# Performance work log

Hardware: AMD Instinct MI355X
Metric: run time of the kernel (lower is better)

Reference implementation:

```python
import jax, jax.numpy as jnp
import numpy as np

HEAD_SIZE = 128
N_Q_HEADS = 32
N_KV_HEADS = 8
ROPE_THETA = 1000000.0
RMS_EPS = 1e-6


def rms_norm(x, w, eps=RMS_EPS):
    # normalize over last dim in fp32, like Qwen3RMSNorm
    xf = x.astype(jnp.float32)
    var = jnp.mean(xf * xf, axis=-1, keepdims=True)
    return w * (xf * jax.lax.rsqrt(var + eps)).astype(x.dtype)


def rope_cache(T, dim, theta=ROPE_THETA):
    half = dim // 2
    inv_freq = 1.0 / theta ** (jnp.arange(half, dtype=jnp.float32) / half)
    freqs = jnp.arange(T, dtype=jnp.float32)[:, None] * inv_freq[None, :]  # [T, half]
    emb = jnp.concatenate([freqs, freqs], axis=-1)  # [T, dim]
    return jnp.cos(emb), jnp.sin(emb)


def rotate_half(x):
    x1, x2 = jnp.split(x, 2, axis=-1)
    return jnp.concatenate([-x2, x1], axis=-1)


def setup_inputs() -> dict:
    key = jax.random.key(0)
    ks = jax.random.split(key, 5)
    B, T, C = 2, 2048, 4096
    s = 0.02
    return {
        "hidden_states": jax.random.normal(ks[0], (B, T, C), jnp.float32),
        "wq": jax.random.normal(ks[1], (N_Q_HEADS * HEAD_SIZE, C), jnp.float32) * s,
        "wk": jax.random.normal(ks[2], (N_KV_HEADS * HEAD_SIZE, C), jnp.float32) * s,
        "wv": jax.random.normal(ks[3], (N_KV_HEADS * HEAD_SIZE, C), jnp.float32) * s,
        "wo": jax.random.normal(ks[4], (C, N_Q_HEADS * HEAD_SIZE), jnp.float32) * s,
        "q_norm_w": jnp.ones((HEAD_SIZE,), jnp.float32),
        "k_norm_w": jnp.ones((HEAD_SIZE,), jnp.float32),
    }


def reference(hidden_states, wq, wk, wv, wo, q_norm_w, k_norm_w):
    B, T, C = hidden_states.shape
    D = HEAD_SIZE
    groups = N_Q_HEADS // N_KV_HEADS
    scale = D ** -0.5

    # projections -> [B, H, T, D]
    q = (hidden_states @ wq.T).reshape(B, T, N_Q_HEADS, D)
    k = (hidden_states @ wk.T).reshape(B, T, N_KV_HEADS, D)
    v = (hidden_states @ wv.T).reshape(B, T, N_KV_HEADS, D)

    q = rms_norm(q, q_norm_w).transpose(0, 2, 1, 3)
    k = rms_norm(k, k_norm_w).transpose(0, 2, 1, 3)
    v = v.transpose(0, 2, 1, 3)

    cos, sin = rope_cache(T, D)  # [T, D]
    cos = cos[None, None]  # broadcast over batch, heads
    sin = sin[None, None]
    q = q * cos + rotate_half(q) * sin
    k = k * cos + rotate_half(k) * sin

    # GQA repeat_kv: [B, Hkv, T, D] -> [B, Hq, T, D]
    k = jnp.repeat(k, groups, axis=1)
    v = jnp.repeat(v, groups, axis=1)

    # causal SDPA
    scores = jnp.einsum("bhqd,bhkd->bhqk", q, k) * scale
    causal = jnp.tril(jnp.ones((T, T), bool))
    scores = jnp.where(causal[None, None], scores, -jnp.inf)
    probs = jax.nn.softmax(scores, axis=-1)
    attn = jnp.einsum("bhqk,bhkd->bhqd", probs, v)

    attn = attn.transpose(0, 2, 1, 3).reshape(B, T, N_Q_HEADS * D)
    return attn @ wo.T
```

## Files before the change

kernel.cpp:

```cpp
#include <hip/hip_runtime.h>
#include <math.h>

typedef unsigned short u16;
typedef __attribute__((ext_vector_type(8))) short short8;
typedef __attribute__((ext_vector_type(4))) float f32x4;
typedef __attribute__((ext_vector_type(16))) float f32x16;

#define AS1 __attribute__((address_space(1)))
#define AS3 __attribute__((address_space(3)))

__device__ __forceinline__ void gload_lds16(const u16* g, u16* l) {
  __builtin_amdgcn_global_load_lds((AS1 void*)g, (AS3 void*)l, 16, 0, 0);
}

__device__ __forceinline__ float bf2f(u16 u) {
  union { unsigned i; float f; } c; c.i = ((unsigned)u) << 16; return c.f;
}
__device__ __forceinline__ u16 f2bf(float f) {
  union { float f; unsigned i; } c; c.f = f;
  unsigned r = c.i + 0x7fffu + ((c.i >> 16) & 1u);
  return (u16)(r >> 16);
}

__global__ __launch_bounds__(256)
void cvt_f32_bf16_k(const float* __restrict__ src, u16* __restrict__ dst, int n8)
{
  int i = blockIdx.x * blockDim.x + threadIdx.x;
  const int stride = gridDim.x * blockDim.x;
  for (; i < n8; i += stride) {
    float4 a = ((const float4*)src)[2 * i];
    float4 b = ((const float4*)src)[2 * i + 1];
    short8 o;
    o[0] = (short)f2bf(a.x); o[1] = (short)f2bf(a.y);
    o[2] = (short)f2bf(a.z); o[3] = (short)f2bf(a.w);
    o[4] = (short)f2bf(b.x); o[5] = (short)f2bf(b.y);
    o[6] = (short)f2bf(b.z); o[7] = (short)f2bf(b.w);
    ((short8*)dst)[i] = o;
  }
}

__global__ __launch_bounds__(256)
void cvt_batch4(const float* __restrict__ s0, u16* __restrict__ d0,
                const float* __restrict__ s1, u16* __restrict__ d1,
                const float* __restrict__ s2, u16* __restrict__ d2,
                const float* __restrict__ s3, u16* __restrict__ d3)
{
  int i = blockIdx.x * blockDim.x + threadIdx.x;
  const int stride = gridDim.x * blockDim.x;
  for (; i < 5242880; i += stride) {
    const float* s; u16* d; int j;
    if (i < 2097152)      { s = s0; d = d0; j = i; }
    else if (i < 4194304) { s = s1; d = d1; j = i - 2097152; }
    else if (i < 4718592) { s = s2; d = d2; j = i - 4194304; }
    else                  { s = s3; d = d3; j = i - 4718592; }
    float4 a = ((const float4*)s)[2 * j];
    float4 b = ((const float4*)s)[2 * j + 1];
    short8 o;
    o[0] = (short)f2bf(a.x); o[1] = (short)f2bf(a.y);
    o[2] = (short)f2bf(a.z); o[3] = (short)f2bf(a.w);
    o[4] = (short)f2bf(b.x); o[5] = (short)f2bf(b.y);
    o[6] = (short)f2bf(b.z); o[7] = (short)f2bf(b.w);
    ((short8*)d)[j] = o;
  }
}

#define MFMA16(a, b, c) __builtin_amdgcn_mfma_f32_16x16x32_bf16((a), (b), (c), 0, 0, 0)

#define STAGE_H(panel, h, t, ldsb)                                          \
  { const u16* s_ = (panel) + (size_t)((h) * 128) * 4096 + (t) * 64;        \
    gload_lds16(s_,                   (ldsb) + ldst0);                      \
    gload_lds16(s_ + (size_t)64*4096, (ldsb) + 4096 + ldst0); }

#define PHASE(MB, STAGE_STMT, TAIL)                                         \
  {                                                                         \
    short8 a0k0 = *(const short8*)(aB + (MB)*1024 + aoff0);                 \
    short8 a0k1 = *(const short8*)(aB + (MB)*1024 + (aoff0 ^ 32));          \
    short8 a1k0 = *(const short8*)(aB + ((MB)+1)*1024 + aoff0);             \
    short8 a1k1 = *(const short8*)(aB + ((MB)+1)*1024 + (aoff0 ^ 32));      \
    __builtin_amdgcn_s_barrier();                                           \
    asm volatile("s_waitcnt lgkmcnt(0)" ::: "memory");                      \
    __builtin_amdgcn_s_setprio(1);                                          \
    _Pragma("unroll")                                                       \
    for (int n = 0; n < 4; ++n) {                                           \
      acc[(MB)][n]   = MFMA16(a0k0, br[n][0], acc[(MB)][n]);                \
      acc[(MB)][n]   = MFMA16(a0k1, br[n][1], acc[(MB)][n]);                \
      acc[(MB)+1][n] = MFMA16(a1k0, br[n][0], acc[(MB)+1][n]);              \
      acc[(MB)+1][n] = MFMA16(a1k1, br[n][1], acc[(MB)+1][n]);              \
    }                                                                       \
    __builtin_amdgcn_s_setprio(0);                                          \
    STAGE_STMT                                                              \
    TAIL                                                                    \
  }

#define KTILE(BUF, T)                                                       \
  {                                                                         \
    const u16* aB = sA + (BUF) * 16384 + wr * 8192;                         \
    const u16* bB = sB + (BUF) * 16384 + (wc >> 1) * 8192;                  \
    u16* aO = sA + ((BUF) ^ 1) * 16384;                                     \
    u16* bO = sB + (BUF) * 16384;                                           \
    const bool st1 = (T) + 1 < NT, st2 = (T) + 2 < NT;                      \
    short8 br[4][2];                                                        \
    _Pragma("unroll")                                                       \
    for (int n = 0; n < 4; ++n) {                                           \
      br[n][0] = *(const short8*)(bB + n * 1024 + boff0);                   \
      br[n][1] = *(const short8*)(bB + n * 1024 + (boff0 ^ 32));            \
    }                                                                       \
    PHASE(0, if (st1) STAGE_H(aS, 0, (T) + 1, aO);, ;)                      \
    PHASE(2, if (st1) STAGE_H(aS, 1, (T) + 1, aO + 8192);, ;)               \
    PHASE(4, if (st2) STAGE_H(bS, 0, (T) + 2, bO);, ;)                      \
    PHASE(6, if (st2) STAGE_H(bS, 1, (T) + 2, bO + 8192);,                  \
          if ((T) < NT - 2) { asm volatile("s_waitcnt vmcnt(4)" ::: "memory"); } \
          else              { asm volatile("s_waitcnt vmcnt(0)" ::: "memory"); } \
          __builtin_amdgcn_s_barrier();)                                    \
  }

template<int MODE, typename OutT>
__global__ __launch_bounds__(512, 2)
void gemm256(const u16* __restrict__ A, const u16* __restrict__ W0,
             const u16* __restrict__ W1, const u16* __restrict__ W2,
             OutT* __restrict__ C)
{
  constexpr int K = 4096;
  constexpr int NT = K / 64;
  constexpr int LDC = (MODE == 0) ? 6144 : 4096;
  constexpr int NBM = 16;
  constexpr int NBN = (MODE == 0) ? 24 : 16;
  constexpr int NWG = NBM * NBN;

  __shared__ __align__(16) u16 sA[2 * 16384];
  __shared__ __align__(16) u16 sB[2 * 16384];

  const int tid = threadIdx.x;
  const int wid = tid >> 6, lane = tid & 63;
  const int g = lane >> 4, li = lane & 15;
  const int wr = wid >> 2, wc = wid & 3;

  const int bid = blockIdx.x;
  const int wg = (bid & 7) * (NWG / 8) + (bid >> 3);
  const int bm = wg % NBM, bn = wg / NBM;
  const int n0 = bn * 256;

  const u16* Wp; int nrow0;
  if (MODE == 0) {
    if (n0 < 4096)      { Wp = W0; nrow0 = n0; }
    else if (n0 < 5120) { Wp = W1; nrow0 = n0 - 4096; }
    else                { Wp = W2; nrow0 = n0 - 5120; }
  } else { Wp = W0; nrow0 = n0; }

  const int r0 = tid >> 3;
  const int sc0 = (tid & 7) ^ (r0 & 7);
  const u16* aS = A  + (size_t)(bm * 256 + r0) * K + sc0 * 8;
  const u16* bS = Wp + (size_t)(nrow0   + r0) * K + sc0 * 8;
  const int ldst0 = wid * 512;

  const int aoff0 = li * 64 + ((g ^ (li & 7)) * 8);
  const int boff0 = (wc & 1) * 4096 + aoff0;

  f32x4 acc[8][4] = {};

  STAGE_H(bS, 0, 0, sB);
  STAGE_H(bS, 1, 0, sB + 8192);
  STAGE_H(aS, 0, 0, sA);
  STAGE_H(aS, 1, 0, sA + 8192);
  STAGE_H(bS, 0, 1, sB + 16384);
  STAGE_H(bS, 1, 1, sB + 24576);
  asm volatile("s_waitcnt vmcnt(4)" ::: "memory");
  __builtin_amdgcn_s_barrier();

  for (int t = 0; t < NT; t += 2) {
    KTILE(0, t)
    KTILE(1, t + 1)
  }

#pragma unroll
  for (int m = 0; m < 8; ++m)
#pragma unroll
    for (int n = 0; n < 4; ++n)
#pragma unroll
      for (int j = 0; j < 4; ++j) {
        int row = bm * 256 + wr * 128 + m * 16 + g * 4 + j;
        int col = n0 + wc * 64 + n * 16 + li;
        float v = acc[m][n][j];
        if constexpr (sizeof(OutT) == 2) C[(size_t)row * LDC + col] = (OutT)f2bf(v);
        else                             C[(size_t)row * LDC + col] = (OutT)v;
      }
}

__global__ __launch_bounds__(256)
void norm_rope(const u16* __restrict__ qkv, const float* __restrict__ qw,
               const float* __restrict__ kw, u16* __restrict__ Qo,
               u16* __restrict__ Ko)
{
  const int tid = threadIdx.x;
  const int wid = tid >> 6, l = tid & 63;
  const int idx = blockIdx.x * 4 + wid;

  const u16* src; const float* w; u16* dst; int t;
  if (idx < 131072) {
    int row = idx >> 5, h = idx & 31;
    int b = row >> 11; t = row & 2047;
    src = qkv + (size_t)row * 6144 + h * 128;
    w = qw;
    dst = Qo + (((size_t)(b * 32 + h)) * 2048 + t) * 128;
  } else {
    int j = idx - 131072;
    int row = j >> 3, hk = j & 7;
    int b = row >> 11; t = row & 2047;
    src = qkv + (size_t)row * 6144 + 4096 + hk * 128;
    w = kw;
    dst = Ko + (((size_t)(b * 8 + hk)) * 2048 + t) * 128;
  }

  float x1 = bf2f(src[l]), x2 = bf2f(src[l + 64]);
  float ss = x1 * x1 + x2 * x2;
#pragma unroll
  for (int off = 32; off; off >>= 1) ss += __shfl_xor(ss, off);
  float rn = rsqrtf(ss * (1.0f / 128.0f) + 1e-6f);
  float y1 = x1 * rn * w[l];
  float y2 = x2 * rn * w[l + 64];

  float ang = (float)t * expf((float)l * -0.21586735246819178f);
  float c = cosf(ang), s = sinf(ang);
  dst[l]      = f2bf(y1 * c - y2 * s);
  dst[l + 64] = f2bf(y2 * c + y1 * s);
}

__global__ __launch_bounds__(256)
void transpose_v(const u16* __restrict__ qkv, u16* __restrict__ Vt)
{
  const int tblk = blockIdx.x, bh = blockIdx.y;
  const int b = bh >> 3, hk = bh & 7;
  const int tid = threadIdx.x;
  __shared__ __align__(16) u16 tile[64][136];

#pragma unroll
  for (int r = 0; r < 4; ++r) {
    int u = tid + r * 256;
    int row = u >> 4, cu = u & 15;
    short8 v = *(const short8*)(qkv + (size_t)(b * 2048 + tblk * 64 + row) * 6144
                                + 5120 + hk * 128 + cu * 8);
    *(short8*)(&tile[row][cu * 8]) = v;
  }
  __syncthreads();
#pragma unroll
  for (int it = 0; it < 4; ++it) {
    int u = tid + it * 256;
    int d = u & 127, tg = u >> 7;
    short8 wv8;
#pragma unroll
    for (int j = 0; j < 8; ++j) wv8[j] = (short)tile[tg * 8 + j][d];
    *(short8*)(Vt + ((size_t)(b * 8 + hk) * 128 + d) * 2048 + tblk * 64 + tg * 8) = wv8;
  }
}

__global__ __launch_bounds__(256, 2)
void attn_fwd(const u16* __restrict__ Q, const u16* __restrict__ Kc,
              const u16* __restrict__ Vt, u16* __restrict__ O)
{
  const int qt = 15 - (int)blockIdx.x;
  const int bh = blockIdx.y;
  const int b = bh >> 5, h = bh & 31, hkv = h >> 2;
  const int tid = threadIdx.x, wid = tid >> 6;
  const int lane = tid & 63, ql = lane & 31, hi = lane >> 5;

  __shared__ __align__(16) u16 sK[2][64 * 128];
  __shared__ __align__(16) u16 sV[2][128 * 64];

  const u16* Kb = Kc + ((size_t)(b * 8 + hkv)) * 2048 * 128;
  const u16* Vb = Vt + ((size_t)(b * 8 + hkv)) * 128 * 2048;

  const int kr0 = tid >> 4;
  const u16* kSrc = Kb + (size_t)kr0 * 128 + (((tid & 15) ^ (kr0 & 7)) * 8);
  const int vr0 = tid >> 3;
  const u16* vSrc = Vb + (size_t)vr0 * 2048 + (((tid & 7) ^ (vr0 & 7)) * 8);
  u16* const kDst = (u16*)sK[0] + wid * 512;
  u16* const vDst = (u16*)sV[0] + wid * 512;

  const int qg = qt * 128 + wid * 32 + ql;
  const u16* qrow = Q + ((size_t)(b * 32 + h) * 2048 + qg) * 128;
  short8 qf[8];
#pragma unroll
  for (int m = 0; m < 8; ++m) qf[m] = *(const short8*)(qrow + m * 16 + hi * 8);

  f32x16 oacc[4] = {};
  float mrun = -INFINITY, lrun = 0.f;
  const float scale = 0.08838834764831845f;
  const int nt = 2 * qt + 2;

#pragma unroll
  for (int p = 0; p < 4; ++p) {
    gload_lds16(kSrc + p * 2048,  kDst + p * 2048);
    gload_lds16(vSrc + p * 65536, vDst + p * 2048);
  }
  asm volatile("s_waitcnt vmcnt(0)" ::: "memory");
  __builtin_amdgcn_s_barrier();

  int cur = 0;
  for (int kt = 0; kt < nt; ++kt) {
    const int kv0 = kt * 64;
    if (kt + 1 < nt) {
      const u16* ks = kSrc + (size_t)(kv0 + 64) * 128;
      const u16* vs = vSrc + (kv0 + 64);
      u16* kd = kDst + (cur ^ 1) * 8192;
      u16* vd = vDst + (cur ^ 1) * 8192;
#pragma unroll
      for (int p = 0; p < 4; ++p) {
        gload_lds16(ks + p * 2048,  kd + p * 2048);
        gload_lds16(vs + p * 65536, vd + p * 2048);
      }
    }
    const u16* sKc = sK[cur];
    const u16* sVc = sV[cur];

    f32x16 P0 = {}, P1 = {};
    __builtin_amdgcn_s_setprio(1);
#pragma unroll
    for (int m = 0; m < 8; ++m) {
      const int c0 = ((m * 2 + hi) ^ (ql & 7)) * 8;
      short8 k0 = *(const short8*)(sKc + ql * 128 + c0);
      short8 k1 = *(const short8*)(sKc + (32 + ql) * 128 + c0);
      P0 = __builtin_amdgcn_mfma_f32_32x32x16_bf16(k0, qf[m], P0, 0, 0, 0);
      P1 = __builtin_amdgcn_mfma_f32_32x32x16_bf16(k1, qf[m], P1, 0, 0, 0);
    }
    __builtin_amdgcn_s_setprio(0);

#pragma unroll
    for (int r = 0; r < 16; ++r) {
      const int kvl = (r & 3) + 8 * (r >> 2) + 4 * hi;
      float v0 = P0[r] * scale; if (kv0 + kvl > qg)      v0 = -INFINITY; P0[r] = v0;
      float v1 = P1[r] * scale; if (kv0 + 32 + kvl > qg) v1 = -INFINITY; P1[r] = v1;
    }

    float pmax = -INFINITY;
#pragma unroll
    for (int r = 0; r < 16; ++r) pmax = fmaxf(pmax, fmaxf(P0[r], P1[r]));
    pmax = fmaxf(pmax, __shfl_xor(pmax, 32));

    if (!__all(pmax - mrun <= 8.f)) {
      float mnew = fmaxf(mrun, pmax);
      float corr = __expf(mrun - mnew);
      lrun *= corr;
      mrun = mnew;
#pragma unroll
      for (int r = 0; r < 16; ++r) {
        int qidx = (r & 3) + 8 * (r >> 2) + 4 * hi;
        float cr = __shfl(corr, qidx);
#pragma unroll
        for (int dt = 0; dt < 4; ++dt) oacc[dt][r] *= cr;
      }
    }

    float psum = 0.f;
#pragma unroll
    for (int r = 0; r < 16; ++r) {
      float e0 = __expf(P0[r] - mrun); P0[r] = e0; psum += e0;
      float e1 = __expf(P1[r] - mrun); P1[r] = e1; psum += e1;
    }
    psum += __shfl_xor(psum, 32);
    lrun += psum;

    __builtin_amdgcn_s_setprio(1);
#pragma unroll
    for (int s = 0; s < 4; ++s) {
      const int R0 = 8 * (s & 1), R1 = R0 + 4;
      float a0 = (s < 2) ? P0[R0 + 0] : P1[R0 + 0];
      float a1 = (s < 2) ? P0[R0 + 1] : P1[R0 + 1];
      float a2 = (s < 2) ? P0[R0 + 2] : P1[R0 + 2];
      float a3 = (s < 2) ? P0[R0 + 3] : P1[R0 + 3];
      float b0 = (s < 2) ? P0[R1 + 0] : P1[R1 + 0];
      float b1 = (s < 2) ? P0[R1 + 1] : P1[R1 + 1];
      float b2 = (s < 2) ? P0[R1 + 2] : P1[R1 + 2];
      float b3 = (s < 2) ? P0[R1 + 3] : P1[R1 + 3];
      unsigned y0, y1, z0, z1;
      asm("v_cvt_pk_bf16_f32 %0, %1, %2" : "=v"(y0) : "v"(a0), "v"(a1));
      asm("v_cvt_pk_bf16_f32 %0, %1, %2" : "=v"(z0) : "v"(b0), "v"(b1));
      asm("v_cvt_pk_bf16_f32 %0, %1, %2" : "=v"(y1) : "v"(a2), "v"(a3));
      asm("v_cvt_pk_bf16_f32 %0, %1, %2" : "=v"(z1) : "v"(b2), "v"(b3));
      asm("v_permlane32_swap_b32 %0, %1" : "+v"(y0), "+v"(z0));
      asm("v_permlane32_swap_b32 %0, %1" : "+v"(y1), "+v"(z1));
      union { unsigned u[4]; short8 v; } pa;
      pa.u[0] = y0; pa.u[1] = y1; pa.u[2] = z0; pa.u[3] = z1;
#pragma unroll
      for (int dt = 0; dt < 4; ++dt) {
        const int c = ((s * 2 + hi) ^ (ql & 7)) * 8;
        short8 vf = *(const short8*)(sVc + (dt * 32 + ql) * 64 + c);
        oacc[dt] = __builtin_amdgcn_mfma_f32_32x32x16_bf16(pa.v, vf, oacc[dt], 0, 0, 0);
      }
    }
    __builtin_amdgcn_s_setprio(0);

    asm volatile("s_waitcnt lgkmcnt(0)" ::: "memory");
    asm volatile("s_waitcnt vmcnt(0)" ::: "memory");
    __builtin_amdgcn_s_barrier();
    cur ^= 1;
  }

  float inv = 1.f / lrun;
  const int qbase = b * 2048 + qt * 128 + wid * 32;
#pragma unroll
  for (int r = 0; r < 16; ++r) {
    const int qidx = (r & 3) + 8 * (r >> 2) + 4 * hi;
    float ir = __shfl(inv, qidx);
    size_t base = (size_t)(qbase + qidx) * 4096 + h * 128 + ql;
#pragma unroll
    for (int dt = 0; dt < 4; ++dt)
      O[base + dt * 32] = f2bf(oacc[dt][r] * ir);
  }
}

extern "C" void kernel_launch(void* const* d_in, const int* in_sizes, int n_in,
                              void* d_out, int out_size, void* d_ws, size_t ws_size,
                              hipStream_t stream) {
  const float* hs  = (const float*)d_in[0];
  const float* wq  = (const float*)d_in[1];
  const float* wk  = (const float*)d_in[2];
  const float* wv  = (const float*)d_in[3];
  const float* wo  = (const float*)d_in[4];
  const float* qnw = (const float*)d_in[5];
  const float* knw = (const float*)d_in[6];
  float* out = (float*)d_out;

  char* ws = (char*)d_ws;
  u16* qkv = (u16*)(ws);
  u16* qr  = (u16*)(ws + 50331648);
  u16* kr  = (u16*)(ws + 83886080);
  u16* vt  = (u16*)(ws + 92274688);
  u16* hsb = (u16*)(ws + 100663296);
  u16* wqb = (u16*)(ws + 134217728);
  u16* wkb = (u16*)(ws + 167772160);
  u16* wvb = (u16*)(ws + 176160768);
  u16* ao  = (u16*)(ws);
  u16* wob = hsb;

  cvt_batch4<<<dim3(2048), dim3(256), 0, stream>>>(hs, hsb, wq, wqb, wk, wkb, wv, wvb);

  gemm256<0, u16><<<dim3(384), dim3(512), 0, stream>>>(hsb, wqb, wkb, wvb, qkv);
  cvt_f32_bf16_k<<<dim3(2048), dim3(256), 0, stream>>>(wo, wob, 16777216 / 8);
  norm_rope<<<dim3(40960), dim3(256), 0, stream>>>(qkv, qnw, knw, qr, kr);
  transpose_v<<<dim3(32, 16), dim3(256), 0, stream>>>(qkv, vt);
  attn_fwd<<<dim3(16, 64), dim3(256), 0, stream>>>(qr, kr, vt, ao);

  gemm256<1, float><<<dim3(256), dim3(512), 0, stream>>>(ao, wob, nullptr, nullptr, out);
}
```

Before: 631.9 us.

## Add 128x256-tile QKV GEMM and restructure stage/barrier ordering in output GEMM

Measured after the change: 626.2 us. No clear change (-0.9%).

```diff
diff --git a/kernel.cpp b/kernel.cpp
--- a/kernel.cpp
+++ b/kernel.cpp
@@ -66,6 +66,130 @@
 
 #define MFMA16(a, b, c) __builtin_amdgcn_mfma_f32_16x16x32_bf16((a), (b), (c), 0, 0, 0)
 
+#define QSTG_A(t, bufb)                                                     \
+  { const u16* s_ = aS + (size_t)(t) * 64;                                  \
+    gload_lds16(s_,                     sA + (bufb) + ldst0);               \
+    gload_lds16(s_ + (size_t)64 * 4096, sA + (bufb) + 4096 + ldst0); }
+
+#define QSTG_B(t, bufb)                                                     \
+  { const u16* s_ = bS + (size_t)(t) * 64;                                  \
+    gload_lds16(s_,                      sB + (bufb) + ldst0);              \
+    gload_lds16(s_ + (size_t)64 * 4096,  sB + (bufb) + 4096 + ldst0);       \
+    gload_lds16(s_ + (size_t)128 * 4096, sB + (bufb) + 8192 + ldst0);       \
+    gload_lds16(s_ + (size_t)192 * 4096, sB + (bufb) + 12288 + ldst0); }
+
+#define QKTILE(BUF, T)                                                      \
+  {                                                                         \
+    const u16* aB = sA + (BUF) * 8192 + wr * 4096;                          \
+    const u16* bB = sB + (BUF) * 16384 + wc * 4096;                         \
+    short8 br[4][2];                                                        \
+    _Pragma("unroll")                                                       \
+    for (int n = 0; n < 4; ++n) {                                           \
+      br[n][0] = *(const short8*)(bB + n * 1024 + qoff0);                   \
+      br[n][1] = *(const short8*)(bB + n * 1024 + (qoff0 ^ 32));            \
+    }                                                                       \
+    {                                                   \
+      short8 a00 = *(const short8*)(aB + qoff0);                            \
+      short8 a01 = *(const short8*)(aB + (qoff0 ^ 32));                     \
+      short8 a10 = *(const short8*)(aB + 1024 + qoff0);                     \
+      short8 a11 = *(const short8*)(aB + 1024 + (qoff0 ^ 32));              \
+      if ((T) + 1 < NT) QSTG_A((T) + 1, ((BUF) ^ 1) * 8192);                \
+      __builtin_amdgcn_s_barrier();                                         \
+      asm volatile("s_waitcnt lgkmcnt(0)" ::: "memory");                    \
+      __builtin_amdgcn_s_setprio(1);                                        \
+      _Pragma("unroll")                                                     \
+      for (int n = 0; n < 4; ++n) {                                         \
+        acc[0][n] = MFMA16(a00, br[n][0], acc[0][n]);                       \
+        acc[0][n] = MFMA16(a01, br[n][1], acc[0][n]);                       \
+        acc[1][n] = MFMA16(a10, br[n][0], acc[1][n]);                       \
+        acc[1][n] = MFMA16(a11, br[n][1], acc[1][n]);                       \
+      }                                                                     \
+      __builtin_amdgcn_s_setprio(0);                                        \
+      __builtin_amdgcn_s_barrier();                                         \
+    }                                                                       \
+    {                                                   \
+      short8 a20 = *(const short8*)(aB + 2048 + qoff0);                     \
+      short8 a21 = *(const short8*)(aB + 2048 + (qoff0 ^ 32));              \
+      short8 a30 = *(const short8*)(aB + 3072 + qoff0);                     \
+      short8 a31 = *(const short8*)(aB + 3072 + (qoff0 ^ 32));              \
+      if ((T) + 2 < NT) QSTG_B((T) + 2, (BUF) * 16384);                     \
+      __builtin_amdgcn_s_barrier();                                         \
+      asm volatile("s_waitcnt lgkmcnt(0)" ::: "memory");                    \
+      __builtin_amdgcn_s_setprio(1);                                        \
+      _Pragma("unroll")                                                     \
+      for (int n = 0; n < 4; ++n) {                                         \
+        acc[2][n] = MFMA16(a20, br[n][0], acc[2][n]);                       \
+        acc[2][n] = MFMA16(a21, br[n][1], acc[2][n]);                       \
+        acc[3][n] = MFMA16(a30, br[n][0], acc[3][n]);                       \
+        acc[3][n] = MFMA16(a31, br[n][1], acc[3][n]);                       \
+      }                                                                     \
+      __builtin_amdgcn_s_setprio(0);                                        \
+      if ((T) < NT - 2) { asm volatile("s_waitcnt vmcnt(4)" ::: "memory"); }\
+      else              { asm volatile("s_waitcnt vmcnt(0)" ::: "memory"); }\
+      __builtin_amdgcn_s_barrier();                                         \
+    }                                                                       \
+  }
+
+__global__ __launch_bounds__(512, 2)
+void gemm_qkv(const u16* __restrict__ A, const u16* __restrict__ W0,
+              const u16* __restrict__ W1, const u16* __restrict__ W2,
+              u16* __restrict__ C)
+{
+  constexpr int K = 4096;
+  constexpr int NT = K / 64;
+  constexpr int NBM = 32, NBN = 24, NWG = NBM * NBN;
+
+  __shared__ __align__(16) u16 sA[2 * 8192];
+  __shared__ __align__(16) u16 sB[2 * 16384];
+
+  const int tid = threadIdx.x;
+  const int wid = tid >> 6, lane = tid & 63;
+  const int g = lane >> 4, li = lane & 15;
+  const int wr = wid >> 2, wc = wid & 3;
+
+  const int bid = blockIdx.x;
+  const int wg = (bid & 7) * (NWG / 8) + (bid >> 3);
+  const int bm = wg % NBM, bn = wg / NBM;
+  const int n0 = bn * 256;
+
+  const u16* Wp; int nrow0;
+  if (n0 < 4096)      { Wp = W0; nrow0 = n0; }
+  else if (n0 < 5120) { Wp = W1; nrow0 = n0 - 4096; }
+  else                { Wp = W2; nrow0 = n0 - 5120; }
+
+  const int r0 = tid >> 3;
+  const int sc0 = (tid & 7) ^ (r0 & 7);
+  const u16* aS = A  + (size_t)(bm * 128 + r0) * K + sc0 * 8;
+  const u16* bS = Wp + (size_t)(nrow0   + r0) * K + sc0 * 8;
+  const int ldst0 = wid * 512;
+
+  const int qoff0 = li * 64 + ((g ^ (li & 7)) * 8);
+
+  f32x4 acc[4][4] = {};
+
+  QSTG_B(0, 0);
+  QSTG_A(0, 0);
+  QSTG_B(1, 16384);
+  asm volatile("s_waitcnt vmcnt(4)" ::: "memory");
+  __builtin_amdgcn_s_barrier();
+
+  for (int t = 0; t < NT; t += 2) {
+    QKTILE(0, t)
+    QKTILE(1, t + 1)
+  }
+
+#pragma unroll
+  for (int m = 0; m < 4; ++m)
+#pragma unroll
+    for (int n = 0; n < 4; ++n)
+#pragma unroll
+      for (int j = 0; j < 4; ++j) {
+        int row = bm * 128 + wr * 64 + m * 16 + g * 4 + j;
+        int col = n0 + wc * 64 + n * 16 + li;
+        C[(size_t)row * 6144 + col] = f2bf(acc[m][n][j]);
+      }
+}
+
 #define STAGE_H(panel, h, t, ldsb)                                          \
   { const u16* s_ = (panel) + (size_t)((h) * 128) * 4096 + (t) * 64;        \
     gload_lds16(s_,                   (ldsb) + ldst0);                      \
@@ -77,6 +201,7 @@
     short8 a0k1 = *(const short8*)(aB + (MB)*1024 + (aoff0 ^ 32));          \
     short8 a1k0 = *(const short8*)(aB + ((MB)+1)*1024 + aoff0);             \
     short8 a1k1 = *(const short8*)(aB + ((MB)+1)*1024 + (aoff0 ^ 32));      \
+    STAGE_STMT                                                              \
     __builtin_amdgcn_s_barrier();                                           \
     asm volatile("s_waitcnt lgkmcnt(0)" ::: "memory");                      \
     __builtin_amdgcn_s_setprio(1);                                          \
@@ -88,8 +213,8 @@
       acc[(MB)+1][n] = MFMA16(a1k1, br[n][1], acc[(MB)+1][n]);              \
     }                                                                       \
     __builtin_amdgcn_s_setprio(0);                                          \
-    STAGE_STMT                                                              \
     TAIL                                                                    \
+    __builtin_amdgcn_s_barrier();                                           \
   }
 
 #define KTILE(BUF, T)                                                       \
@@ -110,22 +235,16 @@
     PHASE(4, if (st2) STAGE_H(bS, 0, (T) + 2, bO);, ;)                      \
     PHASE(6, if (st2) STAGE_H(bS, 1, (T) + 2, bO + 8192);,                  \
           if ((T) < NT - 2) { asm volatile("s_waitcnt vmcnt(4)" ::: "memory"); } \
-          else              { asm volatile("s_waitcnt vmcnt(0)" ::: "memory"); } \
-          __builtin_amdgcn_s_barrier();)                                    \
-  }
-
-template<int MODE, typename OutT>
+          else              { asm volatile("s_waitcnt vmcnt(0)" ::: "memory"); }) \
+  }
+
 __global__ __launch_bounds__(512, 2)
 void gemm256(const u16* __restrict__ A, const u16* __restrict__ W0,
-             const u16* __restrict__ W1, const u16* __restrict__ W2,
-             OutT* __restrict__ C)
+             float* __restrict__ C)
 {
   constexpr int K = 4096;
   constexpr int NT = K / 64;
-  constexpr int LDC = (MODE == 0) ? 6144 : 4096;
-  constexpr int NBM = 16;
-  constexpr int NBN = (MODE == 0) ? 24 : 16;
-  constexpr int NWG = NBM * NBN;
+  constexpr int NBM = 16, NBN = 16, NWG = 256;
 
   __shared__ __align__(16) u16 sA[2 * 16384];
   __shared__ __align__(16) u16 sB[2 * 16384];
@@ -140,17 +259,10 @@
   const int bm = wg % NBM, bn = wg / NBM;
   const int n0 = bn * 256;
 
-  const u16* Wp; int nrow0;
-  if (MODE == 0) {
-    if (n0 < 4096)      { Wp = W0; nrow0 = n0; }
-    else if (n0 < 5120) { Wp = W1; nrow0 = n0 - 4096; }
-    else                { Wp = W2; nrow0 = n0 - 5120; }
-  } else { Wp = W0; nrow0 = n0; }
-
   const int r0 = tid >> 3;
   const int sc0 = (tid & 7) ^ (r0 & 7);
   const u16* aS = A  + (size_t)(bm * 256 + r0) * K + sc0 * 8;
-  const u16* bS = Wp + (size_t)(nrow0   + r0) * K + sc0 * 8;
+  const u16* bS = W0 + (size_t)(n0       + r0) * K + sc0 * 8;
   const int ldst0 = wid * 512;
 
   const int aoff0 = li * 64 + ((g ^ (li & 7)) * 8);
@@ -180,9 +292,7 @@
       for (int j = 0; j < 4; ++j) {
         int row = bm * 256 + wr * 128 + m * 16 + g * 4 + j;
         int col = n0 + wc * 64 + n * 16 + li;
-        float v = acc[m][n][j];
-        if constexpr (sizeof(OutT) == 2) C[(size_t)row * LDC + col] = (OutT)f2bf(v);
-        else                             C[(size_t)row * LDC + col] = (OutT)v;
+        C[(size_t)row * 4096 + col] = acc[m][n][j];
       }
 }
 
@@ -434,11 +544,11 @@
 
   cvt_batch4<<<dim3(2048), dim3(256), 0, stream>>>(hs, hsb, wq, wqb, wk, wkb, wv, wvb);
 
-  gemm256<0, u16><<<dim3(384), dim3(512), 0, stream>>>(hsb, wqb, wkb, wvb, qkv);
+  gemm_qkv<<<dim3(768), dim3(512), 0, stream>>>(hsb, wqb, wkb, wvb, qkv);
   cvt_f32_bf16_k<<<dim3(2048), dim3(256), 0, stream>>>(wo, wob, 16777216 / 8);
   norm_rope<<<dim3(40960), dim3(256), 0, stream>>>(qkv, qnw, knw, qr, kr);
   transpose_v<<<dim3(32, 16), dim3(256), 0, stream>>>(qkv, vt);
   attn_fwd<<<dim3(16, 64), dim3(256), 0, stream>>>(qr, kr, vt, ao);
 
-  gemm256<1, float><<<dim3(256), dim3(512), 0, stream>>>(ao, wob, nullptr, nullptr, out);
-}
+  gemm256<<<dim3(256), dim3(512), 0, stream>>>(ao, wob, out);
+}
```

## Restructure GEMM to 4-wave 128x128 per-wave tiles with simple double buffering

Applied to the files above, without the earlier changes.

Result: slower. 695.8 us (+10.1%).

```diff
diff --git a/kernel.cpp b/kernel.cpp
--- a/kernel.cpp
+++ b/kernel.cpp
@@ -66,59 +66,45 @@
 
 #define MFMA16(a, b, c) __builtin_amdgcn_mfma_f32_16x16x32_bf16((a), (b), (c), 0, 0, 0)
 
-#define STAGE_H(panel, h, t, ldsb)                                          \
-  { const u16* s_ = (panel) + (size_t)((h) * 128) * 4096 + (t) * 64;        \
-    gload_lds16(s_,                   (ldsb) + ldst0);                      \
-    gload_lds16(s_ + (size_t)64*4096, (ldsb) + 4096 + ldst0); }
-
-#define PHASE(MB, STAGE_STMT, TAIL)                                         \
+#define GSTG(panel, T, dst)                                                 \
+  _Pragma("unroll")                                                         \
+  for (int p = 0; p < 8; ++p)                                               \
+    gload_lds16((panel) + (size_t)(p * 32) * 4096 + (size_t)(T) * 64,       \
+                (dst) + p * 2048 + ldst0);
+
+#define GTILE(BUF, T)                                                       \
   {                                                                         \
-    short8 a0k0 = *(const short8*)(aB + (MB)*1024 + aoff0);                 \
-    short8 a0k1 = *(const short8*)(aB + (MB)*1024 + (aoff0 ^ 32));          \
-    short8 a1k0 = *(const short8*)(aB + ((MB)+1)*1024 + aoff0);             \
-    short8 a1k1 = *(const short8*)(aB + ((MB)+1)*1024 + (aoff0 ^ 32));      \
+    const u16* aB = sA + (BUF) * 16384;                                     \
+    const u16* bB = sB + (BUF) * 16384;                                     \
+    short8 af[8][2];                                                        \
+    _Pragma("unroll")                                                       \
+    for (int m = 0; m < 8; ++m) {                                           \
+      af[m][0] = *(const short8*)(aB + aoff0 + m * 1024);                   \
+      af[m][1] = *(const short8*)(aB + (aoff0 ^ 32) + m * 1024);            \
+    }                                                                       \
+    if ((T) + 1 < NT) {                                                     \
+      GSTG(aS, (T) + 1, sA + ((BUF) ^ 1) * 16384)                           \
+      GSTG(bS, (T) + 1, sB + ((BUF) ^ 1) * 16384)                           \
+    }                                                                       \
+    _Pragma("unroll")                                                       \
+    for (int n = 0; n < 8; ++n) {                                           \
+      short8 b0 = *(const short8*)(bB + boff0 + n * 1024);                  \
+      short8 b1 = *(const short8*)(bB + (boff0 ^ 32) + n * 1024);           \
+      _Pragma("unroll")                                                     \
+      for (int m = 0; m < 8; ++m) {                                         \
+        acc[m][n] = MFMA16(af[m][0], b0, acc[m][n]);                        \
+        acc[m][n] = MFMA16(af[m][1], b1, acc[m][n]);                        \
+      }                                                                     \
+    }                                                                       \
+    asm volatile("s_waitcnt vmcnt(0)" ::: "memory");                        \
     __builtin_amdgcn_s_barrier();                                           \
-    asm volatile("s_waitcnt lgkmcnt(0)" ::: "memory");                      \
-    __builtin_amdgcn_s_setprio(1);                                          \
-    _Pragma("unroll")                                                       \
-    for (int n = 0; n < 4; ++n) {                                           \
-      acc[(MB)][n]   = MFMA16(a0k0, br[n][0], acc[(MB)][n]);                \
-      acc[(MB)][n]   = MFMA16(a0k1, br[n][1], acc[(MB)][n]);                \
-      acc[(MB)+1][n] = MFMA16(a1k0, br[n][0], acc[(MB)+1][n]);              \
-      acc[(MB)+1][n] = MFMA16(a1k1, br[n][1], acc[(MB)+1][n]);              \
-    }                                                                       \
-    __builtin_amdgcn_s_setprio(0);                                          \
-    STAGE_STMT                                                              \
-    TAIL                                                                    \
-  }
-
-#define KTILE(BUF, T)                                                       \
-  {                                                                         \
-    const u16* aB = sA + (BUF) * 16384 + wr * 8192;                         \
-    const u16* bB = sB + (BUF) * 16384 + (wc >> 1) * 8192;                  \
-    u16* aO = sA + ((BUF) ^ 1) * 16384;                                     \
-    u16* bO = sB + (BUF) * 16384;                                           \
-    const bool st1 = (T) + 1 < NT, st2 = (T) + 2 < NT;                      \
-    short8 br[4][2];                                                        \
-    _Pragma("unroll")                                                       \
-    for (int n = 0; n < 4; ++n) {                                           \
-      br[n][0] = *(const short8*)(bB + n * 1024 + boff0);                   \
-      br[n][1] = *(const short8*)(bB + n * 1024 + (boff0 ^ 32));            \
-    }                                                                       \
-    PHASE(0, if (st1) STAGE_H(aS, 0, (T) + 1, aO);, ;)                      \
-    PHASE(2, if (st1) STAGE_H(aS, 1, (T) + 1, aO + 8192);, ;)               \
-    PHASE(4, if (st2) STAGE_H(bS, 0, (T) + 2, bO);, ;)                      \
-    PHASE(6, if (st2) STAGE_H(bS, 1, (T) + 2, bO + 8192);,                  \
-          if ((T) < NT - 2) { asm volatile("s_waitcnt vmcnt(4)" ::: "memory"); } \
-          else              { asm volatile("s_waitcnt vmcnt(0)" ::: "memory"); } \
-          __builtin_amdgcn_s_barrier();)                                    \
   }
 
 template<int MODE, typename OutT>
-__global__ __launch_bounds__(512, 2)
-void gemm256(const u16* __restrict__ A, const u16* __restrict__ W0,
-             const u16* __restrict__ W1, const u16* __restrict__ W2,
-             OutT* __restrict__ C)
+__global__ __launch_bounds__(256, 1)
+void gemm_big(const u16* __restrict__ A, const u16* __restrict__ W0,
+              const u16* __restrict__ W1, const u16* __restrict__ W2,
+              OutT* __restrict__ C)
 {
   constexpr int K = 4096;
   constexpr int NT = K / 64;
@@ -133,7 +119,7 @@
   const int tid = threadIdx.x;
   const int wid = tid >> 6, lane = tid & 63;
   const int g = lane >> 4, li = lane & 15;
-  const int wr = wid >> 2, wc = wid & 3;
+  const int wr = wid >> 1, wc = wid & 1;
 
   const int bid = blockIdx.x;
   const int wg = (bid & 7) * (NWG / 8) + (bid >> 3);
@@ -153,33 +139,29 @@
   const u16* bS = Wp + (size_t)(nrow0   + r0) * K + sc0 * 8;
   const int ldst0 = wid * 512;
 
-  const int aoff0 = li * 64 + ((g ^ (li & 7)) * 8);
-  const int boff0 = (wc & 1) * 4096 + aoff0;
-
-  f32x4 acc[8][4] = {};
-
-  STAGE_H(bS, 0, 0, sB);
-  STAGE_H(bS, 1, 0, sB + 8192);
-  STAGE_H(aS, 0, 0, sA);
-  STAGE_H(aS, 1, 0, sA + 8192);
-  STAGE_H(bS, 0, 1, sB + 16384);
-  STAGE_H(bS, 1, 1, sB + 24576);
-  asm volatile("s_waitcnt vmcnt(4)" ::: "memory");
+  const int aoff0 = (wr * 128 + li) * 64 + ((g ^ (li & 7)) * 8);
+  const int boff0 = (wc * 128 + li) * 64 + ((g ^ (li & 7)) * 8);
+
+  f32x4 acc[8][8] = {};
+
+  GSTG(aS, 0, sA)
+  GSTG(bS, 0, sB)
+  asm volatile("s_waitcnt vmcnt(0)" ::: "memory");
   __builtin_amdgcn_s_barrier();
 
   for (int t = 0; t < NT; t += 2) {
-    KTILE(0, t)
-    KTILE(1, t + 1)
+    GTILE(0, t)
+    GTILE(1, t + 1)
   }
 
 #pragma unroll
   for (int m = 0; m < 8; ++m)
 #pragma unroll
-    for (int n = 0; n < 4; ++n)
+    for (int n = 0; n < 8; ++n)
 #pragma unroll
       for (int j = 0; j < 4; ++j) {
         int row = bm * 256 + wr * 128 + m * 16 + g * 4 + j;
-        int col = n0 + wc * 64 + n * 16 + li;
+        int col = n0 + wc * 128 + n * 16 + li;
         float v = acc[m][n][j];
         if constexpr (sizeof(OutT) == 2) C[(size_t)row * LDC + col] = (OutT)f2bf(v);
         else                             C[(size_t)row * LDC + col] = (OutT)v;
@@ -434,11 +416,11 @@
 
   cvt_batch4<<<dim3(2048), dim3(256), 0, stream>>>(hs, hsb, wq, wqb, wk, wkb, wv, wvb);
 
-  gemm256<0, u16><<<dim3(384), dim3(512), 0, stream>>>(hsb, wqb, wkb, wvb, qkv);
+  gemm_big<0, u16><<<dim3(384), dim3(256), 0, stream>>>(hsb, wqb, wkb, wvb, qkv);
   cvt_f32_bf16_k<<<dim3(2048), dim3(256), 0, stream>>>(wo, wob, 16777216 / 8);
   norm_rope<<<dim3(40960), dim3(256), 0, stream>>>(qkv, qnw, knw, qr, kr);
   transpose_v<<<dim3(32, 16), dim3(256), 0, stream>>>(qkv, vt);
   attn_fwd<<<dim3(16, 64), dim3(256), 0, stream>>>(qr, kr, vt, ao);
 
-  gemm256<1, float><<<dim3(256), dim3(512), 0, stream>>>(ao, wob, nullptr, nullptr, out);
-}
+  gemm_big<1, float><<<dim3(256), dim3(256), 0, stream>>>(ao, wob, nullptr, nullptr, out);
+}
```
